# Performance work log

Hardware: AMD Instinct MI355X
Metric: run time of the kernel (lower is better)

## Reference

```python
import jax, jax.numpy as jnp
import numpy as np

HIDDEN = 128
D_T = 128
D_S = 128
EPS = 1e-3  # keras LayerNormalization default epsilon


def setup_inputs() -> dict:
    key = jax.random.key(0)
    ks = jax.random.split(key, 9)
    B, S = 1024, 1024
    h_t = jax.random.normal(ks[0], (B, D_T), dtype=jnp.float32)
    h_s = jax.random.normal(ks[1], (B, S, D_S), dtype=jnp.float32)
    # Dense kernels (keras Dense: y = x @ W + b)
    W_a = jax.random.normal(ks[2], (D_T, HIDDEN), dtype=jnp.float32) * (1.0 / np.sqrt(D_T))
    U_a = jax.random.normal(ks[3], (D_S, HIDDEN), dtype=jnp.float32) * (1.0 / np.sqrt(D_S))
    V_a = jax.random.normal(ks[4], (HIDDEN, 1), dtype=jnp.float32) * (1.0 / np.sqrt(HIDDEN))
    W_c = jax.random.normal(ks[5], (D_S + D_T, HIDDEN), dtype=jnp.float32) * (1.0 / np.sqrt(D_S + D_T))
    b_c = jnp.zeros((HIDDEN,), dtype=jnp.float32)
    gamma = jnp.ones((HIDDEN,), dtype=jnp.float32)
    beta = jnp.zeros((HIDDEN,), dtype=jnp.float32)
    return {"h_t": h_t, "h_s": h_s, "W_a": W_a, "U_a": U_a, "V_a": V_a,
            "W_c": W_c, "b_c": b_c, "gamma": gamma, "beta": beta}


def reference(h_t, h_s, W_a, U_a, V_a, W_c, b_c, gamma, beta):
    # Additive (Bahdanau) attention scores
    ht_proj = h_t @ W_a                              # [B, H]
    hs_proj = jnp.einsum('bsd,dh->bsh', h_s, U_a)    # [B, S, H]
    energy = jnp.tanh(hs_proj + ht_proj[:, None, :])  # [B, S, H]
    scores = jnp.einsum('bsh,ho->bso', energy, V_a)  # [B, S, 1]
    alpha = jax.nn.softmax(scores, axis=1)           # softmax over sequence
    context = jnp.sum(alpha * h_s, axis=1)           # [B, D_S]
    concat = jnp.concatenate([context, h_t], axis=-1)  # [B, D_S + D_T]
    attn_vec = jnp.tanh(concat @ W_c + b_c)          # [B, H]
    # LayerNorm over last axis (keras default eps=1e-3)
    mu = jnp.mean(attn_vec, axis=-1, keepdims=True)
    var = jnp.mean(jnp.square(attn_vec - mu), axis=-1, keepdims=True)
    out = (attn_vec - mu) * jax.lax.rsqrt(var + EPS) * gamma + beta
    return out
```

## Files before the change

### kernel.cpp

```cpp
#include <hip/hip_runtime.h>

#define SEQ 1024
#define NT  16

typedef unsigned short u16;
typedef unsigned int   u32;
typedef __bf16 bf16x8 __attribute__((ext_vector_type(8)));
typedef float  f32x4  __attribute__((ext_vector_type(4)));

__device__ __forceinline__ float fast_tanh(float x) {
    float e = __expf(x + x);
    return 1.0f - 2.0f * __builtin_amdgcn_rcpf(e + 1.0f);
}

#define WAITV(N) do { asm volatile("s_waitcnt vmcnt(" #N ")" ::: "memory"); \
                      __builtin_amdgcn_sched_barrier(0); } while (0)

#define LOADT(rr, tt)                                                        \
    do {                                                                     \
        int rowb = ((tt)*64 + w*16 + lo)*32 + hi*2;                          \
        _Pragma("unroll")                                                    \
        for (int ks = 0; ks < 4; ++ks) {                                     \
            rr[2*ks]   = hs4[rowb + ks*8];                                   \
            rr[2*ks+1] = hs4[rowb + ks*8 + 1];                               \
        }                                                                    \
    } while (0)

#define CVT8(dst, vlo, vhi)                                                  \
    { dst[0]=(__bf16)(vlo)[0]; dst[1]=(__bf16)(vlo)[1];                      \
      dst[2]=(__bf16)(vlo)[2]; dst[3]=(__bf16)(vlo)[3];                      \
      dst[4]=(__bf16)(vhi)[0]; dst[5]=(__bf16)(vhi)[1];                      \
      dst[6]=(__bf16)(vhi)[2]; dst[7]=(__bf16)(vhi)[3]; }

#define BF(n, ks) (*(const bf16x8*)&Ut[(n)*2048 + lo*128 + ((((ks)*4+hi) ^ lo) << 3)])

#define NSTEP(n)                                                             \
    do {                                                                     \
        f32x4 acc = {0.f, 0.f, 0.f, 0.f};                                    \
        acc = __builtin_amdgcn_mfma_f32_16x16x32_bf16(aa0, BF(n,0), acc, 0, 0, 0); \
        acc = __builtin_amdgcn_mfma_f32_16x16x32_bf16(aa1, BF(n,1), acc, 0, 0, 0); \
        acc = __builtin_amdgcn_mfma_f32_16x16x32_bf16(aa2, BF(n,2), acc, 0, 0, 0); \
        acc = __builtin_amdgcn_mfma_f32_16x16x32_bf16(aa3, BF(n,3), acc, 0, 0, 0); \
        float hC = htpR[n], vC = VsR[n];                                     \
        part0 += fast_tanh(acc[0] + hC) * vC;                                \
        part1 += fast_tanh(acc[1] + hC) * vC;                                \
        part2 += fast_tanh(acc[2] + hC) * vC;                                \
        part3 += fast_tanh(acc[3] + hC) * vC;                                \
    } while (0)

#define COMPUTE(rr)                                                          \
    do {                                                                     \
        bf16x8 aa0, aa1, aa2, aa3;                                           \
        CVT8(aa0, rr[0], rr[1]); CVT8(aa1, rr[2], rr[3]);                    \
        CVT8(aa2, rr[4], rr[5]); CVT8(aa3, rr[6], rr[7]);                    \
        float part0 = 0.f, part1 = 0.f, part2 = 0.f, part3 = 0.f;            \
        NSTEP(0); NSTEP(1); NSTEP(2); NSTEP(3);                              \
        NSTEP(4); NSTEP(5); NSTEP(6); NSTEP(7);                              \
        _Pragma("unroll")                                                    \
        for (int msk = 1; msk < 16; msk <<= 1) {                             \
            part0 += __shfl_xor(part0, msk);                                 \
            part1 += __shfl_xor(part1, msk);                                 \
            part2 += __shfl_xor(part2, msk);                                 \
            part3 += __shfl_xor(part3, msk);                                 \
        }                                                                    \
        float e0 = __expf(part0), e1 = __expf(part1);                        \
        float e2 = __expf(part2), e3 = __expf(part3);                        \
        lsum += e0 + e1 + e2 + e3;                                           \
        if (lo == 0) {                                                       \
            redArr[w*16 + hi*4 + 0] = e0;                                    \
            redArr[w*16 + hi*4 + 1] = e1;                                    \
            redArr[w*16 + hi*4 + 2] = e2;                                    \
            redArr[w*16 + hi*4 + 3] = e3;                                    \
        }                                                                    \
        float wr = redArr[w*16 + lo];         \
        _Pragma("unroll")                                                    \
        for (int i = 0; i < 8; ++i) c_part[i] += wr * rr[i];                 \
    } while (0)

__global__ __launch_bounds__(256) __attribute__((amdgpu_waves_per_eu(2, 2)))
void attn_fused(const float* __restrict__ h_t, const float* __restrict__ h_s,
                const float* __restrict__ W_a, const float* __restrict__ U_a,
                const float* __restrict__ V_a, const float* __restrict__ W_c,
                const float* __restrict__ b_c, const float* __restrict__ gamma,
                const float* __restrict__ beta, float* __restrict__ out)
{
    __shared__ u16 Ut[128*128];
    __shared__ float htp[128];
    __shared__ float htrow[128];
    __shared__ float redArr[64];
    __shared__ float cw[512];
    __shared__ float lw[4], lnp[4], lnq[4];

    const int tid = threadIdx.x;
    const int b   = blockIdx.x;
    const int w   = tid >> 6, l = tid & 63;
    const int lo  = l & 15,  hi = l >> 4;

    const f32x4* hs4 = (const f32x4*)(h_s + (size_t)b * (SEQ*128));

    f32x4 rrA[8], rrB[8];
    LOADT(rrA, 0);
    LOADT(rrB, 1);

    if (tid < 128) htrow[tid] = h_t[b*128 + tid];

    const float4* U4 = (const float4*)U_a;
    #pragma unroll
    for (int i = 0; i < 16; ++i) {
        int f4i = i*256 + tid;
        float4 v = U4[f4i];
        int k  = f4i >> 5;
        int cb = (f4i & 31) * 4;
        float vv[4] = {v.x, v.y, v.z, v.w};
        #pragma unroll
        for (int j = 0; j < 4; ++j) {
            int c = cb + j;
            Ut[c*128 + (((k>>3) ^ (c&15)) << 3) + (k&7)] = __builtin_bit_cast(u16, (__bf16)vv[j]);
        }
    }
    __syncthreads();

    if (tid < 128) {
        float acc = 0.f;
        #pragma unroll 4
        for (int d = 0; d < 128; ++d) acc += htrow[d] * W_a[d*128 + tid];
        htp[tid] = acc;
    }
    __syncthreads();

    float htpR[8], VsR[8];
    #pragma unroll
    for (int n = 0; n < 8; ++n) { htpR[n] = htp[n*16 + lo]; VsR[n] = V_a[n*16 + lo]; }

    float lsum = 0.f;
    f32x4 c_part[8];
    #pragma unroll
    for (int i = 0; i < 8; ++i) c_part[i] = (f32x4){0.f, 0.f, 0.f, 0.f};

    for (int t = 0; t < NT-2; t += 2) {
        WAITV(8);  COMPUTE(rrA);  LOADT(rrA, t+2);
        WAITV(8);  COMPUTE(rrB);  LOADT(rrB, t+3);
    }
    WAITV(8);  COMPUTE(rrA);
    WAITV(0);  COMPUTE(rrB);

    #pragma unroll
    for (int i = 0; i < 8; ++i) {
        #pragma unroll
        for (int msk = 1; msk < 16; msk <<= 1) {
            c_part[i][0] += __shfl_xor(c_part[i][0], msk);
            c_part[i][1] += __shfl_xor(c_part[i][1], msk);
            c_part[i][2] += __shfl_xor(c_part[i][2], msk);
            c_part[i][3] += __shfl_xor(c_part[i][3], msk);
        }
    }
    float lt = lsum;
    lt += __shfl_xor(lt, 16);
    lt += __shfl_xor(lt, 32);
    if (l == 0) lw[w] = lt;
    if (lo == 0) {
        #pragma unroll
        for (int i = 0; i < 8; ++i)
            *(f32x4*)&cw[w*128 + (i>>1)*32 + hi*8 + (i&1)*4] = c_part[i];
    }
    __syncthreads();

    if (tid < 128) {
        float L = lw[0] + lw[1] + lw[2] + lw[3];
        float C = cw[tid] + cw[128 + tid] + cw[256 + tid] + cw[384 + tid];
        htp[tid] = C / L;
    }
    __syncthreads();

    float av = 0.f;
    if (tid < 128) {
        float acc = b_c[tid];
        #pragma unroll 4
        for (int k = 0; k < 128; ++k) acc += htp[k]   * W_c[k*128 + tid];
        #pragma unroll 4
        for (int k = 0; k < 128; ++k) acc += htrow[k] * W_c[(128 + k)*128 + tid];
        av = fast_tanh(acc);
    }
    float s1 = (tid < 128) ? av : 0.f;
    #pragma unroll
    for (int msk = 1; msk < 64; msk <<= 1) s1 += __shfl_xor(s1, msk);
    if (l == 0) lnp[w] = s1;
    __syncthreads();
    float mu  = (lnp[0] + lnp[1]) * (1.f/128.f);
    float dev = av - mu;
    float s2 = (tid < 128) ? dev*dev : 0.f;
    #pragma unroll
    for (int msk = 1; msk < 64; msk <<= 1) s2 += __shfl_xor(s2, msk);
    if (l == 0) lnq[w] = s2;
    __syncthreads();
    float var = (lnq[0] + lnq[1]) * (1.f/128.f);
    if (tid < 128) {
        out[b*128 + tid] = dev * rsqrtf(var + 1e-3f) * gamma[tid] + beta[tid];
    }
}

extern "C" void kernel_launch(void* const* d_in, const int* in_sizes, int n_in,
                              void* d_out, int out_size, void* d_ws, size_t ws_size,
                              hipStream_t stream) {
    const float* h_t  = (const float*)d_in[0];
    const float* h_s  = (const float*)d_in[1];
    const float* W_a  = (const float*)d_in[2];
    const float* U_a  = (const float*)d_in[3];
    const float* V_a  = (const float*)d_in[4];
    const float* W_c  = (const float*)d_in[5];
    const float* b_c  = (const float*)d_in[6];
    const float* gam  = (const float*)d_in[7];
    const float* bet  = (const float*)d_in[8];
    float* out = (float*)d_out;
    hipLaunchKernelGGL(attn_fused, dim3(1024), dim3(256), 0, stream,
                       h_t, h_s, W_a, U_a, V_a, W_c, b_c, gam, bet, out);
}
```

Measured before the change: 156.8 us.

## Single-buffer tile loads, fold bias into MFMA, shuffle weights, raise occupancy

Replaces the double-buffered register tiles with a single buffer. The tile is converted to bf16 right away and the next load is issued immediately, which frees registers so occupancy can go up to 3 waves per EU. The ht projection bias is folded into the MFMA accumulator's initial value. The LDS redArr round trip for the softmax weights is replaced by a cross-lane shuffle. Context accumulation now uses the bf16-rounded inputs instead of fp32, which slightly lowers precision, and setprio is added around the MFMA section.

```diff
diff --git a/kernel.cpp b/kernel.cpp
--- a/kernel.cpp
+++ b/kernel.cpp
@@ -13,10 +13,7 @@
     return 1.0f - 2.0f * __builtin_amdgcn_rcpf(e + 1.0f);
 }
 
-#define WAITV(N) do { asm volatile("s_waitcnt vmcnt(" #N ")" ::: "memory"); \
-                      __builtin_amdgcn_sched_barrier(0); } while (0)
-
-#define LOADT(rr, tt)                                                        \
+#define LOADT(tt)                                                            \
     do {                                                                     \
         int rowb = ((tt)*64 + w*16 + lo)*32 + hi*2;                          \
         _Pragma("unroll")                                                    \
@@ -32,30 +29,40 @@
       dst[4]=(__bf16)(vhi)[0]; dst[5]=(__bf16)(vhi)[1];                      \
       dst[6]=(__bf16)(vhi)[2]; dst[7]=(__bf16)(vhi)[3]; }
 
+#define CVTALL                                                               \
+    CVT8(aa0, rr[0], rr[1]); CVT8(aa1, rr[2], rr[3]);                        \
+    CVT8(aa2, rr[4], rr[5]); CVT8(aa3, rr[6], rr[7]);
+
 #define BF(n, ks) (*(const bf16x8*)&Ut[(n)*2048 + lo*128 + ((((ks)*4+hi) ^ lo) << 3)])
 
 #define NSTEP(n)                                                             \
     do {                                                                     \
-        f32x4 acc = {0.f, 0.f, 0.f, 0.f};                                    \
+        float hC = htpR[n];                                                  \
+        f32x4 acc = {hC, hC, hC, hC};                                        \
         acc = __builtin_amdgcn_mfma_f32_16x16x32_bf16(aa0, BF(n,0), acc, 0, 0, 0); \
         acc = __builtin_amdgcn_mfma_f32_16x16x32_bf16(aa1, BF(n,1), acc, 0, 0, 0); \
         acc = __builtin_amdgcn_mfma_f32_16x16x32_bf16(aa2, BF(n,2), acc, 0, 0, 0); \
         acc = __builtin_amdgcn_mfma_f32_16x16x32_bf16(aa3, BF(n,3), acc, 0, 0, 0); \
-        float hC = htpR[n], vC = VsR[n];                                     \
-        part0 += fast_tanh(acc[0] + hC) * vC;                                \
-        part1 += fast_tanh(acc[1] + hC) * vC;                                \
-        part2 += fast_tanh(acc[2] + hC) * vC;                                \
-        part3 += fast_tanh(acc[3] + hC) * vC;                                \
+        float vC = VsR[n];                                                   \
+        part0 += fast_tanh(acc[0]) * vC;                                     \
+        part1 += fast_tanh(acc[1]) * vC;                                     \
+        part2 += fast_tanh(acc[2]) * vC;                                     \
+        part3 += fast_tanh(acc[3]) * vC;                                     \
     } while (0)
 
-#define COMPUTE(rr)                                                          \
+#define CTX(ks, AA)                                                          \
+    { f32x4 t0 = {(float)AA[0], (float)AA[1], (float)AA[2], (float)AA[3]};   \
+      f32x4 t1 = {(float)AA[4], (float)AA[5], (float)AA[6], (float)AA[7]};   \
+      c_part[2*(ks)]   += wr * t0;                                           \
+      c_part[2*(ks)+1] += wr * t1; }
+
+#define REST                                                                 \
     do {                                                                     \
-        bf16x8 aa0, aa1, aa2, aa3;                                           \
-        CVT8(aa0, rr[0], rr[1]); CVT8(aa1, rr[2], rr[3]);                    \
-        CVT8(aa2, rr[4], rr[5]); CVT8(aa3, rr[6], rr[7]);                    \
         float part0 = 0.f, part1 = 0.f, part2 = 0.f, part3 = 0.f;            \
+        __builtin_amdgcn_s_setprio(1);                                       \
         NSTEP(0); NSTEP(1); NSTEP(2); NSTEP(3);                              \
         NSTEP(4); NSTEP(5); NSTEP(6); NSTEP(7);                              \
+        __builtin_amdgcn_s_setprio(0);                                       \
         _Pragma("unroll")                                                    \
         for (int msk = 1; msk < 16; msk <<= 1) {                             \
             part0 += __shfl_xor(part0, msk);                                 \
@@ -66,18 +73,14 @@
         float e0 = __expf(part0), e1 = __expf(part1);                        \
         float e2 = __expf(part2), e3 = __expf(part3);                        \
         lsum += e0 + e1 + e2 + e3;                                           \
-        if (lo == 0) {                                                       \
-            redArr[w*16 + hi*4 + 0] = e0;                                    \
-            redArr[w*16 + hi*4 + 1] = e1;                                    \
-            redArr[w*16 + hi*4 + 2] = e2;                                    \
-            redArr[w*16 + hi*4 + 3] = e3;                                    \
-        }                                                                    \
-        float wr = redArr[w*16 + lo];         \
-        _Pragma("unroll")                                                    \
-        for (int i = 0; i < 8; ++i) c_part[i] += wr * rr[i];                 \
+             \
+        float sel = (lo & 2) ? ((lo & 1) ? e3 : e2)                          \
+                             : ((lo & 1) ? e1 : e0);                         \
+        float wr  = __shfl(sel, (lo >> 2) * 16 + (lo & 3), 64);              \
+        CTX(0, aa0); CTX(1, aa1); CTX(2, aa2); CTX(3, aa3);                  \
     } while (0)
 
-__global__ __launch_bounds__(256) __attribute__((amdgpu_waves_per_eu(2, 2)))
+__global__ __launch_bounds__(256) __attribute__((amdgpu_waves_per_eu(3)))
 void attn_fused(const float* __restrict__ h_t, const float* __restrict__ h_s,
                 const float* __restrict__ W_a, const float* __restrict__ U_a,
                 const float* __restrict__ V_a, const float* __restrict__ W_c,
@@ -87,7 +90,6 @@
     __shared__ u16 Ut[128*128];
     __shared__ float htp[128];
     __shared__ float htrow[128];
-    __shared__ float redArr[64];
     __shared__ float cw[512];
     __shared__ float lw[4], lnp[4], lnq[4];
 
@@ -98,9 +100,8 @@
 
     const f32x4* hs4 = (const f32x4*)(h_s + (size_t)b * (SEQ*128));
 
-    f32x4 rrA[8], rrB[8];
-    LOADT(rrA, 0);
-    LOADT(rrB, 1);
+    f32x4 rr[8];
+    LOADT(0);
 
     if (tid < 128) htrow[tid] = h_t[b*128 + tid];
 
@@ -137,12 +138,17 @@
     #pragma unroll
     for (int i = 0; i < 8; ++i) c_part[i] = (f32x4){0.f, 0.f, 0.f, 0.f};
 
-    for (int t = 0; t < NT-2; t += 2) {
-        WAITV(8);  COMPUTE(rrA);  LOADT(rrA, t+2);
-        WAITV(8);  COMPUTE(rrB);  LOADT(rrB, t+3);
-    }
-    WAITV(8);  COMPUTE(rrA);
-    WAITV(0);  COMPUTE(rrB);
+    for (int t = 0; t < NT-1; ++t) {
+        bf16x8 aa0, aa1, aa2, aa3;
+        CVTALL;
+        LOADT(t+1);
+        REST;
+    }
+    {
+        bf16x8 aa0, aa1, aa2, aa3;
+        CVTALL;
+        REST;
+    }
 
     #pragma unroll
     for (int i = 0; i < 8; ++i) {
```

After: 553.0 us. 253% more time.
